# Kernel optimization log

Measured on AMD Instinct MI355X. Metric: run time of the kernel, lower is better.

The kernel has to match this reference:

```python
import jax, jax.numpy as jnp
import numpy as np

BN_EPS = 1e-5

def _haar_details(x):
    # pywt.dwt2(x, 'haar') details for even H, W.
    # Block [[p, q], [r, s]] with p = x[2i,2j], q = x[2i,2j+1], r = x[2i+1,2j], s = x[2i+1,2j+1].
    # cH ('da'): detail along rows, approx along cols; cV ('ad'); cD ('dd').
    B, C, H, W = x.shape
    xb = x.reshape(B, C, H // 2, 2, W // 2, 2)
    p = xb[:, :, :, 0, :, 0]
    q = xb[:, :, :, 0, :, 1]
    r = xb[:, :, :, 1, :, 0]
    s = xb[:, :, :, 1, :, 1]
    cH = (p + q - r - s) * 0.5
    cV = (p - q + r - s) * 0.5
    cD = (p - q - r + s) * 0.5
    return cH, cV, cD

def setup_inputs() -> dict:
    key = jax.random.key(0)
    k1, k2 = jax.random.split(key)
    B, C, H, W = 8, 256, 128, 128
    x = jax.random.normal(k1, (B, C, H, W), dtype=jnp.float32)
    conv_w = jax.random.normal(k2, (C, 4 * C), dtype=jnp.float32) * (1.0 / np.sqrt(4 * C))
    gamma = jnp.ones((C,), dtype=jnp.float32)
    beta = jnp.zeros((C,), dtype=jnp.float32)
    return {"x": x, "conv_w": conv_w, "gamma": gamma, "beta": beta}

def reference(x, conv_w, gamma, beta):
    B, C, H, W = x.shape
    # Original detaches the wavelet branch (CPU numpy path) -> stop_gradient.
    xs = jax.lax.stop_gradient(x)
    cH, cV, cD = _haar_details(xs)
    # Bilinear upsample to (H, W); jax.image.resize bilinear == torch align_corners=False.
    up = lambda t: jax.image.resize(t, (B, C, H, W), method="bilinear")
    enhanced = jnp.concatenate([x, up(cH), up(cV), up(cD)], axis=1)  # [B, 4C, H, W]
    # 1x1 conv, no bias.
    y = jnp.einsum("bchw,oc->bohw", enhanced, conv_w)  # [B, C, H, W]
    # BatchNorm2d, training-mode (batch statistics, biased variance).
    mean = jnp.mean(y, axis=(0, 2, 3), keepdims=True)
    var = jnp.mean((y - mean) ** 2, axis=(0, 2, 3), keepdims=True)
    y_hat = (y - mean) * jax.lax.rsqrt(var + BN_EPS)
    out = jax.nn.relu(y_hat * gamma[None, :, None, None] + beta[None, :, None, None])
    return out
```

## Files before the change

### kernel.cpp

```cpp
#include <hip/hip_runtime.h>
#include <hip/hip_bf16.h>

typedef __bf16 bf16;
typedef __bf16 bf16x4 __attribute__((ext_vector_type(4)));
typedef __bf16 bf16x8 __attribute__((ext_vector_type(8)));
typedef float  f32x4  __attribute__((ext_vector_type(4)));

#define AS1 __attribute__((address_space(1)))
#define AS3 __attribute__((address_space(3)))

__device__ __forceinline__ void load16_to_lds(const bf16* g, bf16* l) {
    __builtin_amdgcn_global_load_lds((const AS1 unsigned int*)g,
                                     (AS3 unsigned int*)l, 16, 0, 0);
}

__global__ __launch_bounds__(256) void prep_w(const float* __restrict__ w,
                                              bf16* __restrict__ wb) {
    int idx = (blockIdx.x * 256 + threadIdx.x) * 4;
    const float4 v = *(const float4*)(w + idx);
    bf16x4 o; o[0]=(bf16)v.x; o[1]=(bf16)v.y; o[2]=(bf16)v.z; o[3]=(bf16)v.w;
    *(bf16x4*)(wb + idx) = o;
}

__device__ __forceinline__ int tix(int row, int chunk, int lo) {
    return row * 264 + (((chunk ^ ((row >> 2) & 7)) << 3) | lo);
}

__global__ __launch_bounds__(256, 4) void fused_x(const float* __restrict__ x,
                                                  const bf16* __restrict__ W,
                                                  bf16* __restrict__ cT,
                                                  bf16* __restrict__ y1) {
    __shared__ bf16 tile[64 * 264];
    const int bid = blockIdx.x;
    const int wt = bid & 3, j = (bid >> 2) & 63, b = bid >> 8;
    const int t = threadIdx.x;
    const int w0 = wt * 32;
    const int wave = t >> 6, lane = t & 63;
    const int quad = lane >> 4, l16 = lane & 15;
    const int wo = wave * 64;

    bf16x8 wf_cur[4], wf_nxt[4];
    #pragma unroll
    for (int jj = 0; jj < 4; ++jj)
        wf_cur[jj] = *(const bf16x8*)(W +
            (size_t)(wo + jj * 16 + l16) * 1024 + quad * 8);

    float4 v[16];
    #pragma unroll
    for (int i = 0; i < 16; ++i) {
        int g = i * 256 + t;
        int c = g >> 4, rem = g & 15;
        int dlt = rem >> 3, w4 = rem & 7;
        v[i] = *(const float4*)(x +
            ((((size_t)b * 256 + c) * 128 + (2 * j + dlt)) * 128 + w0 + w4 * 4));
    }
    #pragma unroll
    for (int i = 0; i < 16; ++i) {
        int g = i * 256 + t;
        int c = g >> 4, rem = g & 15;
        int dlt = rem >> 3, w4 = rem & 7;
        int pos = dlt * 32 + w4 * 4;
        int cs = tix(pos, c >> 3, c & 7) - pos * 264;
        tile[(pos + 0) * 264 + cs] = (bf16)v[i].x;
        tile[(pos + 1) * 264 + cs] = (bf16)v[i].y;
        tile[(pos + 2) * 264 + cs] = (bf16)v[i].z;
        tile[(pos + 3) * 264 + cs] = (bf16)v[i].w;
    }
    __syncthreads();

    for (int i = 0; i < 2; ++i) {
        int q = i * 256 + t;
        int cq = q & 31, kc = q >> 5;
        int r0 = 2 * kc, r1 = 2 * kc + 1, r2 = 32 + 2 * kc, r3 = 33 + 2 * kc;
        bf16x8 vp = *(const bf16x8*)&tile[tix(r0, cq, 0)];
        bf16x8 vq = *(const bf16x8*)&tile[tix(r1, cq, 0)];
        bf16x8 vr = *(const bf16x8*)&tile[tix(r2, cq, 0)];
        bf16x8 vs = *(const bf16x8*)&tile[tix(r3, cq, 0)];
        bf16x8 oh, ov, od;
        #pragma unroll
        for (int e = 0; e < 8; ++e) {
            float p = (float)vp[e], qq = (float)vq[e];
            float r = (float)vr[e], s = (float)vs[e];
            oh[e] = (bf16)(0.5f * (p + qq - r - s));
            ov[e] = (bf16)(0.5f * (p - qq + r - s));
            od[e] = (bf16)(0.5f * (p - qq - r + s));
        }
        size_t row = ((size_t)b * 4096 + j * 64 + wt * 16 + kc) * 768;
        *(bf16x8*)(cT + row + 0 * 256 + cq * 8) = oh;
        *(bf16x8*)(cT + row + 1 * 256 + cq * 8) = ov;
        *(bf16x8*)(cT + row + 2 * 256 + cq * 8) = od;
    }

    f32x4 acc[4][4] = {};
    #pragma unroll
    for (int kk = 0; kk < 256; kk += 32) {
        if (kk < 224) {
            #pragma unroll
            for (int jj = 0; jj < 4; ++jj)
                wf_nxt[jj] = *(const bf16x8*)(W +
                    (size_t)(wo + jj * 16 + l16) * 1024 + kk + 32 + quad * 8);
        }
        bf16x8 xf[4];
        #pragma unroll
        for (int i2 = 0; i2 < 4; ++i2)
            xf[i2] = *(const bf16x8*)&tile[tix(i2 * 16 + l16,
                                               (kk >> 3) + quad, 0)];
        #pragma unroll
        for (int i2 = 0; i2 < 4; ++i2)
            #pragma unroll
            for (int jj = 0; jj < 4; ++jj)
                acc[i2][jj] = __builtin_amdgcn_mfma_f32_16x16x32_bf16(
                    xf[i2], wf_cur[jj], acc[i2][jj], 0, 0, 0);
        #pragma unroll
        for (int jj = 0; jj < 4; ++jj) wf_cur[jj] = wf_nxt[jj];
    }

    #pragma unroll
    for (int i = 0; i < 4; ++i) {
        int p = i * 16 + quad * 4;
        int h = 2 * j + (p >> 5), wc = w0 + (p & 31);
        #pragma unroll
        for (int jj = 0; jj < 4; ++jj) {
            int o = wo + jj * 16 + l16;
            bf16x4 vv;
            #pragma unroll
            for (int r = 0; r < 4; ++r) vv[r] = (bf16)acc[i][jj][r];
            *(bf16x4*)(y1 + ((size_t)b * 256 + o) * 16384 + h * 128 + wc) = vv;
        }
    }
}

__global__ __launch_bounds__(256, 4) void gemm2(const bf16* __restrict__ W,
                                                const bf16* __restrict__ cT,
                                                bf16* __restrict__ z) {
    __shared__ bf16 Xt[128 * 32];
    const int bid = blockIdx.x;
    const int m0 = (bid & 255) * 128, o0 = (bid >> 8) * 128;
    const int t = threadIdx.x;
    const int wave = t >> 6, lane = t & 63;
    const int quad = lane >> 4, l16 = lane & 15;
    const int wo = (wave >> 1) * 64, wm = (wave & 1) * 64;
    const int r_in = lane >> 2, cch = lane & 3;

    f32x4 acc[4][4] = {};
    const bf16* wbase = W + (size_t)o0 * 1024 + 256;
    const bf16* xbase = cT + (size_t)m0 * 768;

    bf16x8 af_cur[4], af_nxt[4];
    #pragma unroll
    for (int i = 0; i < 4; ++i)
        af_cur[i] = *(const bf16x8*)(wbase +
            (size_t)(wo + i * 16 + l16) * 1024 + quad * 8);

    #pragma unroll 2
    for (int kk = 0; kk < 768; kk += 32) {
        #pragma unroll
        for (int i = 0; i < 2; ++i) {
            int rblk = wave * 2 + i;
            int row = rblk * 16 + r_in;
            load16_to_lds(xbase + (size_t)row * 768 + kk + cch * 8,
                          &Xt[rblk * 512 + lane * 8]);
        }
        __syncthreads();
        if (kk < 736) {
            #pragma unroll
            for (int i = 0; i < 4; ++i)
                af_nxt[i] = *(const bf16x8*)(wbase +
                    (size_t)(wo + i * 16 + l16) * 1024 + kk + 32 + quad * 8);
        }
        bf16x8 bfr[4];
        #pragma unroll
        for (int jj = 0; jj < 4; ++jj)
            bfr[jj] = *(const bf16x8*)&Xt[(wm + jj * 16 + l16) * 32 + quad * 8];
        #pragma unroll
        for (int i = 0; i < 4; ++i)
            #pragma unroll
            for (int jj = 0; jj < 4; ++jj)
                acc[i][jj] = __builtin_amdgcn_mfma_f32_16x16x32_bf16(
                    bfr[jj], af_cur[i], acc[i][jj], 0, 0, 0);
        __syncthreads();
        #pragma unroll
        for (int i = 0; i < 4; ++i) af_cur[i] = af_nxt[i];
    }

    #pragma unroll
    for (int i = 0; i < 4; ++i) {
        int o = o0 + wo + i * 16 + l16;
        #pragma unroll
        for (int jj = 0; jj < 4; ++jj) {
            int m = m0 + wm + jj * 16 + quad * 4;
            int bb = m >> 12, mp = m & 4095;
            bf16x4 vv;
            #pragma unroll
            for (int r = 0; r < 4; ++r) vv[r] = (bf16)acc[i][jj][r];
            *(bf16x4*)(z + ((size_t)bb * 256 + o) * 4096 + mp) = vv;
        }
    }
}

__device__ __forceinline__ void load_zplane(const bf16* zp, float* zs, int t) {
    for (int i = 0; i < 2; ++i) {
        int idx = (i * 256 + t) * 8;
        int j = idx >> 6, k = idx & 63;
        bf16x8 v = *(const bf16x8*)(zp + idx);
        #pragma unroll
        for (int e = 0; e < 8; ++e) zs[j * 65 + k + e] = (float)v[e];
    }
}

__device__ __forceinline__ void up8(const float* zs, int base, float* u) {
    int h = base >> 7, w0 = base & 127;
    int j0 = h >> 1;
    int jn = (h & 1) ? min(j0 + 1, 63) : max(j0 - 1, 0);
    int K = w0 >> 1;
    float z0[6], z1[6];
    #pragma unroll
    for (int d = 0; d < 6; ++d) {
        int kc = min(max(K - 1 + d, 0), 63);
        z0[d] = zs[j0 * 65 + kc];
        z1[d] = zs[jn * 65 + kc];
    }
    #pragma unroll
    for (int e = 0; e < 8; ++e) {
        int a = (e >> 1) + 1;
        int bb = (e & 1) ? a + 1 : a - 1;
        u[e] = 0.5625f * z0[a] + 0.1875f * (z0[bb] + z1[a]) + 0.0625f * z1[bb];
    }
}

__global__ __launch_bounds__(256) void stats_k(const bf16* __restrict__ y1,
                                               const bf16* __restrict__ z,
                                               float* __restrict__ stats) {
    __shared__ float zs[64 * 65];
    __shared__ float red[8];
    const int bid = blockIdx.x;
    const int o = bid & 255, b = bid >> 8;
    const int t = threadIdx.x;
    const bf16* zp = z + ((size_t)b * 256 + o) * 4096;
    const bf16* yp = y1 + ((size_t)b * 256 + o) * 16384;
    load_zplane(zp, zs, t);
    __syncthreads();
    float s = 0.f, ss = 0.f;
    for (int i = 0; i < 8; ++i) {
        int base = (i * 256 + t) * 8;
        float u[8];
        up8(zs, base, u);
        bf16x8 yv = *(const bf16x8*)(yp + base);
        #pragma unroll
        for (int e = 0; e < 8; ++e) {
            float y = (float)yv[e] + u[e];
            s += y; ss += y * y;
        }
    }
    #pragma unroll
    for (int off = 32; off > 0; off >>= 1) {
        s += __shfl_down(s, off);
        ss += __shfl_down(ss, off);
    }
    if ((t & 63) == 0) { red[t >> 6] = s; red[4 + (t >> 6)] = ss; }
    __syncthreads();
    if (t == 0) {
        atomicAdd(&stats[o],       red[0] + red[1] + red[2] + red[3]);
        atomicAdd(&stats[256 + o], red[4] + red[5] + red[6] + red[7]);
    }
}

__global__ __launch_bounds__(256) void finalize_k(float* __restrict__ stats,
                                                  const float* __restrict__ gamma,
                                                  const float* __restrict__ beta) {
    int o = threadIdx.x;
    const float n = 131072.f;
    float mean = stats[o] / n;
    float var = stats[256 + o] / n - mean * mean;
    float rstd = rsqrtf(var + 1e-5f);
    float sc = rstd * gamma[o];
    stats[512 + o] = sc;
    stats[768 + o] = beta[o] - mean * sc;
}

__global__ __launch_bounds__(256) void apply_k(const bf16* __restrict__ y1,
                                               const bf16* __restrict__ z,
                                               const float* __restrict__ stats,
                                               float* __restrict__ out) {
    __shared__ float zs[64 * 65];
    const int bid = blockIdx.x;
    const int o = bid & 255, b = bid >> 8;
    const int t = threadIdx.x;
    const bf16* zp = z + ((size_t)b * 256 + o) * 4096;
    const bf16* yp = y1 + ((size_t)b * 256 + o) * 16384;
    float* op = out + ((size_t)b * 256 + o) * 16384;
    const float sc = stats[512 + o], sh = stats[768 + o];
    load_zplane(zp, zs, t);
    __syncthreads();
    for (int i = 0; i < 8; ++i) {
        int base = (i * 256 + t) * 8;
        float u[8];
        up8(zs, base, u);
        bf16x8 yv = *(const bf16x8*)(yp + base);
        float4 o0, o1;
        o0.x = fmaxf(fmaf((float)yv[0] + u[0], sc, sh), 0.f);
        o0.y = fmaxf(fmaf((float)yv[1] + u[1], sc, sh), 0.f);
        o0.z = fmaxf(fmaf((float)yv[2] + u[2], sc, sh), 0.f);
        o0.w = fmaxf(fmaf((float)yv[3] + u[3], sc, sh), 0.f);
        o1.x = fmaxf(fmaf((float)yv[4] + u[4], sc, sh), 0.f);
        o1.y = fmaxf(fmaf((float)yv[5] + u[5], sc, sh), 0.f);
        o1.z = fmaxf(fmaf((float)yv[6] + u[6], sc, sh), 0.f);
        o1.w = fmaxf(fmaf((float)yv[7] + u[7], sc, sh), 0.f);
        *(float4*)(op + base) = o0;
        *(float4*)(op + base + 4) = o1;
    }
}

extern "C" void kernel_launch(void* const* d_in, const int* in_sizes, int n_in,
                              void* d_out, int out_size, void* d_ws, size_t ws_size,
                              hipStream_t stream) {
    const float* x      = (const float*)d_in[0];
    const float* conv_w = (const float*)d_in[1];
    const float* gamma  = (const float*)d_in[2];
    const float* beta   = (const float*)d_in[3];
    float* out = (float*)d_out;

    char* ws = (char*)d_ws;
    bf16*  Wbf   = (bf16*)ws;
    bf16*  z     = (bf16*)(ws + (512ll << 10));
    float* stats = (float*)(ws + (512ll << 10) + (16ll << 20));
    bf16*  cT    = (bf16*)(ws + (512ll << 10) + (16ll << 20) + 4096);
    bf16*  y1    = (bf16*)(ws + (512ll << 10) + (64ll << 20) + 4096);

    hipMemsetAsync(stats, 0, 4096, stream);
    prep_w<<<256, 256, 0, stream>>>(conv_w, Wbf);
    fused_x<<<2048, 256, 0, stream>>>(x, Wbf, cT, y1);
    gemm2<<<512, 256, 0, stream>>>(Wbf, cT, z);
    stats_k<<<2048, 256, 0, stream>>>(y1, z, stats);
    finalize_k<<<1, 256, 0, stream>>>(stats, gamma, beta);
    apply_k<<<2048, 256, 0, stream>>>(y1, z, stats, out);
}
```

Baseline: 401.8 us.

## Split x staging into halves, relax launch bounds, fold BN finalize into apply

The x-tile load in fused_x is split into two halves of 8 float4 loads to cut register pressure, and its launch-bounds minimum occupancy drops from 4 to 2 blocks. gemm2 loses its occupancy hint and its unroll-2 pragma. The separate single-block finalize kernel is removed, and each apply_k block computes scale and shift from the stats itself, saving one launch at the cost of redundant per-block arithmetic. Splitting the load reduces memory-level parallelism, and the lower occupancy target may hurt latency hiding.

```diff
diff --git a/kernel.cpp b/kernel.cpp
--- a/kernel.cpp
+++ b/kernel.cpp
@@ -26,7 +26,7 @@
     return row * 264 + (((chunk ^ ((row >> 2) & 7)) << 3) | lo);
 }
 
-__global__ __launch_bounds__(256, 4) void fused_x(const float* __restrict__ x,
+__global__ __launch_bounds__(256, 2) void fused_x(const float* __restrict__ x,
                                                   const bf16* __restrict__ W,
                                                   bf16* __restrict__ cT,
                                                   bf16* __restrict__ y1) {
@@ -39,43 +39,47 @@
     const int quad = lane >> 4, l16 = lane & 15;
     const int wo = wave * 64;
 
+    #pragma unroll
+    for (int half = 0; half < 2; ++half) {
+        float4 v[8];
+        #pragma unroll
+        for (int i = 0; i < 8; ++i) {
+            int g = (half * 8 + i) * 256 + t;
+            int c = g >> 4, rem = g & 15;
+            int dlt = rem >> 3, w4 = rem & 7;
+            v[i] = *(const float4*)(x +
+                ((((size_t)b * 256 + c) * 128 + (2 * j + dlt)) * 128 + w0 + w4 * 4));
+        }
+        #pragma unroll
+        for (int i = 0; i < 8; ++i) {
+            int g = (half * 8 + i) * 256 + t;
+            int c = g >> 4, rem = g & 15;
+            int dlt = rem >> 3, w4 = rem & 7;
+            int pos = dlt * 32 + w4 * 4;
+            int cs = tix(pos, c >> 3, c & 7) - pos * 264;
+            tile[(pos + 0) * 264 + cs] = (bf16)v[i].x;
+            tile[(pos + 1) * 264 + cs] = (bf16)v[i].y;
+            tile[(pos + 2) * 264 + cs] = (bf16)v[i].z;
+            tile[(pos + 3) * 264 + cs] = (bf16)v[i].w;
+        }
+    }
+
     bf16x8 wf_cur[4], wf_nxt[4];
     #pragma unroll
     for (int jj = 0; jj < 4; ++jj)
         wf_cur[jj] = *(const bf16x8*)(W +
             (size_t)(wo + jj * 16 + l16) * 1024 + quad * 8);
 
-    float4 v[16];
-    #pragma unroll
-    for (int i = 0; i < 16; ++i) {
-        int g = i * 256 + t;
-        int c = g >> 4, rem = g & 15;
-        int dlt = rem >> 3, w4 = rem & 7;
-        v[i] = *(const float4*)(x +
-            ((((size_t)b * 256 + c) * 128 + (2 * j + dlt)) * 128 + w0 + w4 * 4));
-    }
-    #pragma unroll
-    for (int i = 0; i < 16; ++i) {
-        int g = i * 256 + t;
-        int c = g >> 4, rem = g & 15;
-        int dlt = rem >> 3, w4 = rem & 7;
-        int pos = dlt * 32 + w4 * 4;
-        int cs = tix(pos, c >> 3, c & 7) - pos * 264;
-        tile[(pos + 0) * 264 + cs] = (bf16)v[i].x;
-        tile[(pos + 1) * 264 + cs] = (bf16)v[i].y;
-        tile[(pos + 2) * 264 + cs] = (bf16)v[i].z;
-        tile[(pos + 3) * 264 + cs] = (bf16)v[i].w;
-    }
     __syncthreads();
 
+    #pragma unroll
     for (int i = 0; i < 2; ++i) {
         int q = i * 256 + t;
         int cq = q & 31, kc = q >> 5;
-        int r0 = 2 * kc, r1 = 2 * kc + 1, r2 = 32 + 2 * kc, r3 = 33 + 2 * kc;
-        bf16x8 vp = *(const bf16x8*)&tile[tix(r0, cq, 0)];
-        bf16x8 vq = *(const bf16x8*)&tile[tix(r1, cq, 0)];
-        bf16x8 vr = *(const bf16x8*)&tile[tix(r2, cq, 0)];
-        bf16x8 vs = *(const bf16x8*)&tile[tix(r3, cq, 0)];
+        bf16x8 vp = *(const bf16x8*)&tile[tix(2 * kc, cq, 0)];
+        bf16x8 vq = *(const bf16x8*)&tile[tix(2 * kc + 1, cq, 0)];
+        bf16x8 vr = *(const bf16x8*)&tile[tix(32 + 2 * kc, cq, 0)];
+        bf16x8 vs = *(const bf16x8*)&tile[tix(33 + 2 * kc, cq, 0)];
         bf16x8 oh, ov, od;
         #pragma unroll
         for (int e = 0; e < 8; ++e) {
@@ -130,9 +134,9 @@
     }
 }
 
-__global__ __launch_bounds__(256, 4) void gemm2(const bf16* __restrict__ W,
-                                                const bf16* __restrict__ cT,
-                                                bf16* __restrict__ z) {
+__global__ __launch_bounds__(256) void gemm2(const bf16* __restrict__ W,
+                                             const bf16* __restrict__ cT,
+                                             bf16* __restrict__ z) {
     __shared__ bf16 Xt[128 * 32];
     const int bid = blockIdx.x;
     const int m0 = (bid & 255) * 128, o0 = (bid >> 8) * 128;
@@ -152,7 +156,6 @@
         af_cur[i] = *(const bf16x8*)(wbase +
             (size_t)(wo + i * 16 + l16) * 1024 + quad * 8);
 
-    #pragma unroll 2
     for (int kk = 0; kk < 768; kk += 32) {
         #pragma unroll
         for (int i = 0; i < 2; ++i) {
@@ -265,22 +268,11 @@
     }
 }
 
-__global__ __launch_bounds__(256) void finalize_k(float* __restrict__ stats,
-                                                  const float* __restrict__ gamma,
-                                                  const float* __restrict__ beta) {
-    int o = threadIdx.x;
-    const float n = 131072.f;
-    float mean = stats[o] / n;
-    float var = stats[256 + o] / n - mean * mean;
-    float rstd = rsqrtf(var + 1e-5f);
-    float sc = rstd * gamma[o];
-    stats[512 + o] = sc;
-    stats[768 + o] = beta[o] - mean * sc;
-}
-
 __global__ __launch_bounds__(256) void apply_k(const bf16* __restrict__ y1,
                                                const bf16* __restrict__ z,
                                                const float* __restrict__ stats,
+                                               const float* __restrict__ gamma,
+                                               const float* __restrict__ beta,
                                                float* __restrict__ out) {
     __shared__ float zs[64 * 65];
     const int bid = blockIdx.x;
@@ -289,7 +281,11 @@
     const bf16* zp = z + ((size_t)b * 256 + o) * 4096;
     const bf16* yp = y1 + ((size_t)b * 256 + o) * 16384;
     float* op = out + ((size_t)b * 256 + o) * 16384;
-    const float sc = stats[512 + o], sh = stats[768 + o];
+    const float n = 131072.f;
+    float mean = stats[o] / n;
+    float var = stats[256 + o] / n - mean * mean;
+    float sc = rsqrtf(var + 1e-5f) * gamma[o];
+    float sh = beta[o] - mean * sc;
     load_zplane(zp, zs, t);
     __syncthreads();
     for (int i = 0; i < 8; ++i) {
@@ -332,6 +328,5 @@
     fused_x<<<2048, 256, 0, stream>>>(x, Wbf, cT, y1);
     gemm2<<<512, 256, 0, stream>>>(Wbf, cT, z);
     stats_k<<<2048, 256, 0, stream>>>(y1, z, stats);
-    finalize_k<<<1, 256, 0, stream>>>(stats, gamma, beta);
-    apply_k<<<2048, 256, 0, stream>>>(y1, z, stats, out);
-}
+    apply_k<<<2048, 256, 0, stream>>>(y1, z, stats, gamma, beta, out);
+}
```

After: 346.7 us. 1.16x faster.
